# Performance work log

Measured on AMD Instinct MI355X. Metric: run time of the kernel, lower is better.

The kernel has to match this reference:

```python
import jax, jax.numpy as jnp
import numpy as np

B, D, C, H = 32768, 128, 128, 512
INTERVAL = 1.0
N_STEPS = 4
ENERGY_REG = 0.01
JACNORM_REG = 0.01


def setup_inputs() -> dict:
    key = jax.random.key(0)
    ks = jax.random.split(key, 8)
    return {
        "x": jax.random.normal(ks[0], (B, D), jnp.float32),
        "logpx": jnp.zeros((B,), jnp.float32),
        "cond": jax.random.normal(ks[1], (B, C), jnp.float32),
        "e": jax.random.normal(ks[2], (B, D), jnp.float32),  # Hutchinson noise
        "W1": jax.random.normal(ks[3], (D, H), jnp.float32) / np.sqrt(D),
        "Wc": jax.random.normal(ks[4], (C, H), jnp.float32) / np.sqrt(C),
        "bt": jax.random.normal(ks[5], (H,), jnp.float32) * 0.1,
        "b1": jnp.zeros((H,), jnp.float32),
        "W2": jax.random.normal(ks[6], (H, D), jnp.float32) / np.sqrt(H),
        "b2": jnp.zeros((D,), jnp.float32),
    }


def reference(x, logpx, cond, e, W1, Wc, bt, b1, W2, b2):
    def drift(t, xx):
        # func(t, x, cond): simple conditioned MLP drift
        h = jnp.tanh(xx @ W1 + cond @ Wc + t * bt + b1)
        return h @ W2 + b2

    def dynamics(t, xx):
        # Hutchinson divergence estimator: div = e^T (dF/dx) e via one VJP
        dx, vjp_fn = jax.vjp(lambda z: drift(t, z), xx)
        u = vjp_fn(e)[0]                      # [B, D] = e^T J
        div = jnp.sum(u * e, axis=1)          # [B]
        d_energy = jnp.sum(dx * dx) / xx.shape[0]
        d_jacnorm = jnp.sum(u * u) / xx.shape[0]
        return dx, -div, d_energy, d_jacnorm

    dt = INTERVAL / N_STEPS

    def rk4_step(carry, t0):
        xx, lp, en, jn = carry
        k1 = dynamics(t0, xx)
        k2 = dynamics(t0 + 0.5 * dt, xx + 0.5 * dt * k1[0])
        k3 = dynamics(t0 + 0.5 * dt, xx + 0.5 * dt * k2[0])
        k4 = dynamics(t0 + dt, xx + dt * k3[0])
        comb = lambda i: (k1[i] + 2.0 * k2[i] + 2.0 * k3[i] + k4[i]) / 6.0
        return (xx + dt * comb(0), lp + dt * comb(1), en + dt * comb(2), jn + dt * comb(3)), None

    ts = jnp.arange(N_STEPS, dtype=x.dtype) * dt
    init = (x, logpx, jnp.zeros((), x.dtype), jnp.zeros((), x.dtype))
    (y, logpy, energy, jacnorm), _ = jax.lax.scan(rk4_step, init, ts)

    # regularization: zero value, nonzero gradient (matches x - x.detach())
    reg = ENERGY_REG * (energy - jax.lax.stop_gradient(energy)) \
        + JACNORM_REG * (jacnorm - jax.lax.stop_gradient(jacnorm))
    return y, logpy + reg
```

## Files before the change

### kernel.cpp

```cpp
#include <hip/hip_runtime.h>

typedef unsigned short u16;
typedef unsigned int   u32;
typedef unsigned long long u64;
typedef __attribute__((ext_vector_type(8))) short bf16x8;
typedef __attribute__((ext_vector_type(4))) float f32x4;

#define MFMA16(A,B,C) __builtin_amdgcn_mfma_f32_16x16x32_bf16(A,B,C,0,0,0)
#define MFMAF8(A,B,C) __builtin_amdgcn_mfma_f32_16x16x32_fp8_fp8(A,B,C,0,0,0)

__device__ __forceinline__ u16 f2bf(float f){
    u32 u = __float_as_uint(f);
    u += 0x7fffu + ((u >> 16) & 1u);
    return (u16)(u >> 16);
}
__device__ __forceinline__ u32 pk2(float lo, float hi){
    return (u32)f2bf(lo) | ((u32)f2bf(hi) << 16);
}
__device__ __forceinline__ float upk(u32 u, int hi){
    return __uint_as_float(hi ? (u & 0xffff0000u) : (u << 16));
}
__device__ __forceinline__ float bf2f(u16 v){
    return __uint_as_float(((u32)v) << 16);
}
__device__ __forceinline__ float fast_tanh(float p){
    float e2 = __expf(2.f * p);
    return 1.f - __fdividef(2.f, e2 + 1.f);
}
__device__ __forceinline__ void gload16(const u16* g, u16* l){
    __builtin_amdgcn_global_load_lds((const __attribute__((address_space(1))) void*)g,
                                     (__attribute__((address_space(3))) void*)l, 16, 0, 0);
}

__global__ __launch_bounds__(256) void pack_weights_kernel(
    const float* __restrict__ W1, const float* __restrict__ W2,
    const float* __restrict__ Wc, u16* __restrict__ wp)
{
    int p = blockIdx.x * 256 + threadIdx.x;
    int which = p >> 16;
    int q = p & 65535;
    if (which == 1) return;
    if (which == 2){
        int j = q & 7, lane = (q >> 3) & 63;
        int nt = (q >> 9) & 7, lc = (q >> 12) & 15;
        int k = lc * 32 + (lane >> 4) * 8 + j;
        int n = nt * 16 + (lane & 15);
        float v = W2[k * 128 + n];
        u32 b = (u32)__builtin_amdgcn_cvt_pk_fp8_f32(v, 0.f, 0, 0) & 0xffu;
        ((unsigned char*)(wp + 131072))[q] = (unsigned char)b;
        return;
    }
    int j = q & 7, l = (q >> 3) & 63, t = (q >> 9) & 1;
    int ks = (q >> 10) & 3, c = (q >> 12) & 15;
    int l15v = l & 15, l4v = l >> 4;
    int k = 32 * ks + l4v * 8 + j;
    int n = 32 * c + 16 * t + l15v;
    float v = (which == 0) ? W1[k * 512 + n] : (which == 3) ? W2[n * 128 + k] : Wc[k * 512 + n];
    wp[p] = f2bf(v);
}

__global__ __launch_bounds__(512, 4) void cnf_mfma11_kernel(
    const float* __restrict__ x, const float* __restrict__ logpx,
    const float* __restrict__ cond, const float* __restrict__ e,
    const float* __restrict__ b1, const u16* __restrict__ wp,
    const float* __restrict__ bt, const float* __restrict__ b2,
    float* __restrict__ y_out, float* __restrict__ lp_out)
{
    __shared__ __align__(16) u16 s_w1[3][4096];
    __shared__ __align__(16) unsigned char s_w2s[4][4096];
    __shared__ __align__(16) u16 s_xx[4][16 * 136];
    __shared__ __align__(16) unsigned char s_hh8[4][2][16 * 40];
    __shared__ u16 s_bt[512];
    __shared__ float s_b2[128];
    __shared__ float s_red[4][2][16];

    const int tid = threadIdx.x, wave = tid >> 6, lane = tid & 63;
    const int l15 = lane & 15, l4 = lane >> 4;
    const int pair = wave >> 1, half = wave & 1;
    const int rbase = blockIdx.x * 64 + pair * 16;
    const int wlt4 = __builtin_amdgcn_readfirstlane((wave < 4) ? 1 : 0);

    const u16* W1p  = wp;
    const u16* W2Tp = wp + 196608;
    const u16* Wcp  = wp + 262144;
    const unsigned char* W2f8p = (const unsigned char*)(wp + 131072);

    auto stage_chunk = [&](int slot, int slot4, int cidx){
        gload16(W1p + cidx * 4096 + wave * 512 + lane * 8, &s_w1[slot][wave * 512 + lane * 8]);
        if (wave < 4)
            gload16((const u16*)(W2f8p + cidx * 4096 + wave * 1024 + lane * 16),
                    (u16*)&s_w2s[slot4][wave * 1024 + lane * 16]);
    };

    s_bt[tid] = f2bf(bt[tid]);
    if (tid < 128) s_b2[tid] = b2[tid];

    u32 base_pk[16][2], q_pk[16][2];

    {
        #pragma unroll
        for (int i = 0; i < 8; ++i){
            const int row = half * 8 + i;
            s_xx[pair][row * 136 + lane]      = f2bf(cond[(size_t)(rbase + row) * 128 + lane]);
            s_xx[pair][row * 136 + 64 + lane] = f2bf(cond[(size_t)(rbase + row) * 128 + 64 + lane]);
        }
        __syncthreads();
        bf16x8 cA[4];
        #pragma unroll
        for (int ks = 0; ks < 4; ++ks)
            cA[ks] = *(const bf16x8*)&s_xx[pair][l15 * 136 + ks * 32 + l4 * 8];
        __syncthreads();

        #pragma unroll 1
        for (int nc = 0; nc < 16; ++nc){
            gload16(Wcp + nc * 4096 + wave * 512 + lane * 8, &s_w1[0][wave * 512 + lane * 8]);
            __syncthreads();
            f32x4 ab = {0.f, 0.f, 0.f, 0.f};
            #pragma unroll
            for (int ks = 0; ks < 4; ++ks)
                ab = MFMA16(cA[ks], *(const bf16x8*)&s_w1[0][(ks * 2 + half) * 512 + lane * 8], ab);
            const float b1v = b1[nc * 32 + half * 16 + l15];
            base_pk[nc][0] = pk2(ab[0] + b1v, ab[1] + b1v);
            base_pk[nc][1] = pk2(ab[2] + b1v, ab[3] + b1v);
            __syncthreads();
        }
    }

    {
        #pragma unroll
        for (int i = 0; i < 8; ++i){
            const int row = half * 8 + i;
            s_xx[pair][row * 136 + lane]      = f2bf(e[(size_t)(rbase + row) * 128 + lane]);
            s_xx[pair][row * 136 + 64 + lane] = f2bf(e[(size_t)(rbase + row) * 128 + 64 + lane]);
        }
        __syncthreads();
        bf16x8 eA[4];
        #pragma unroll
        for (int ks = 0; ks < 4; ++ks)
            eA[ks] = *(const bf16x8*)&s_xx[pair][l15 * 136 + ks * 32 + l4 * 8];
        __syncthreads();

        #pragma unroll 1
        for (int nc = 0; nc < 16; ++nc){
            gload16(W1p  + nc * 4096 + wave * 512 + lane * 8, &s_w1[0][wave * 512 + lane * 8]);
            gload16(W2Tp + nc * 4096 + wave * 512 + lane * 8, &s_w1[1][wave * 512 + lane * 8]);
            __syncthreads();
            f32x4 ew = {0.f,0.f,0.f,0.f}, e2 = {0.f,0.f,0.f,0.f};
            #pragma unroll
            for (int ks = 0; ks < 4; ++ks){
                ew = MFMA16(eA[ks], *(const bf16x8*)&s_w1[0][(ks * 2 + half) * 512 + lane * 8], ew);
                e2 = MFMA16(eA[ks], *(const bf16x8*)&s_w1[1][(ks * 2 + half) * 512 + lane * 8], e2);
            }
            q_pk[nc][0] = pk2(ew[0] * e2[0], ew[1] * e2[1]);
            q_pk[nc][1] = pk2(ew[2] * e2[2], ew[3] * e2[3]);
            __syncthreads();
        }
    }

    u32 xs_pk[4][2];
    #pragma unroll
    for (int ntl = 0; ntl < 4; ++ntl)
        #pragma unroll
        for (int rr = 0; rr < 2; ++rr){
            const int row0 = rbase + l4 * 4 + 2 * rr;
            const int col = half * 64 + ntl * 16 + l15;
            const float a0 = x[(size_t)row0 * 128 + col];
            const float a1 = x[(size_t)(row0 + 1) * 128 + col];
            xs_pk[ntl][rr] = pk2(a0, a1);
            s_xx[pair][(l4 * 4 + 2 * rr) * 136 + col]     = (u16)(xs_pk[ntl][rr] & 0xffffu);
            s_xx[pair][(l4 * 4 + 2 * rr + 1) * 136 + col] = (u16)(xs_pk[ntl][rr] >> 16);
        }

    #pragma unroll
    for (int c = 0; c < 3; ++c) stage_chunk(c, c, c);
    if (wlt4) { asm volatile("s_waitcnt vmcnt(4) lgkmcnt(0)" ::: "memory"); }
    else      { asm volatile("s_waitcnt vmcnt(2) lgkmcnt(0)" ::: "memory"); }
    __builtin_amdgcn_sched_barrier(0);
    __builtin_amdgcn_s_barrier();
    asm volatile("" ::: "memory");

    f32x4 acc[4];
    u32 dxc_pk[4][2];
    float divacc[4] = {0.f, 0.f, 0.f, 0.f};
    #pragma unroll
    for (int ntl = 0; ntl < 4; ++ntl){
        acc[ntl] = {0.f, 0.f, 0.f, 0.f};
        dxc_pk[ntl][0] = 0u; dxc_pk[ntl][1] = 0u;
    }

    #pragma unroll 1
    for (int st = 0; st < 16; ++st){
        const int stg = st & 3;
        const float tcur = 0.25f * (float)(st >> 2) + ((stg == 0) ? 0.f : (stg == 3) ? 0.25f : 0.125f);
        const float wcur = (stg == 1 || stg == 2) ? 2.f : 1.f;

        #pragma unroll 1
        for (int lc = 0; lc < 16; ++lc){
            const int c = st * 16 + lc;
            const int slot = c % 3;

            {
                const float btv = bf2f(s_bt[lc * 32 + half * 16 + l15]);
                f32x4 pa, pb = {0.f, 0.f, 0.f, 0.f};
                pa[0] = upk(base_pk[lc][0], 0) + tcur * btv;
                pa[1] = upk(base_pk[lc][0], 1) + tcur * btv;
                pa[2] = upk(base_pk[lc][1], 0) + tcur * btv;
                pa[3] = upk(base_pk[lc][1], 1) + tcur * btv;
                bf16x8 xxA0 = *(const bf16x8*)&s_xx[pair][l15 * 136 +  0 + l4 * 8];
                bf16x8 xxA1 = *(const bf16x8*)&s_xx[pair][l15 * 136 + 32 + l4 * 8];
                bf16x8 xxA2 = *(const bf16x8*)&s_xx[pair][l15 * 136 + 64 + l4 * 8];
                bf16x8 xxA3 = *(const bf16x8*)&s_xx[pair][l15 * 136 + 96 + l4 * 8];
                pa = MFMA16(xxA0, *(const bf16x8*)&s_w1[slot][(0 * 2 + half) * 512 + lane * 8], pa);
                pb = MFMA16(xxA1, *(const bf16x8*)&s_w1[slot][(1 * 2 + half) * 512 + lane * 8], pb);
                pa = MFMA16(xxA2, *(const bf16x8*)&s_w1[slot][(2 * 2 + half) * 512 + lane * 8], pa);
                pb = MFMA16(xxA3, *(const bf16x8*)&s_w1[slot][(3 * 2 + half) * 512 + lane * 8], pb);
                #pragma unroll
                for (int r = 0; r < 4; ++r){
                    const float h = fast_tanh(pa[r] + pb[r]);
                    divacc[r] += wcur * (1.f - h * h) * upk(q_pk[lc][r >> 1], r & 1);
                    const u32 hb = (u32)__builtin_amdgcn_cvt_pk_fp8_f32(h, h, 0, 0) & 0xffu;
                    s_hh8[pair][c & 1][(l4 * 4 + r) * 40 + half * 16 + l15] = (unsigned char)hb;
                }
            }

            if (wlt4) { asm volatile("s_waitcnt vmcnt(2) lgkmcnt(0)" ::: "memory"); }
            else      { asm volatile("s_waitcnt vmcnt(1) lgkmcnt(0)" ::: "memory"); }
            __builtin_amdgcn_sched_barrier(0);
            __builtin_amdgcn_s_barrier();
            asm volatile("" ::: "memory");

            stage_chunk((c + 3) % 3, (c + 3) & 3, (c + 3) & 15);

            {
                const u64 hf8 = *(const u64*)&s_hh8[pair][c & 1][l15 * 40 + l4 * 8];
                #pragma unroll
                for (int ntl = 0; ntl < 4; ++ntl){
                    const u64 wf8 = *(const u64*)&s_w2s[c & 3][(half * 4 + ntl) * 512 + lane * 8];
                    acc[ntl] = MFMAF8((long)hf8, (long)wf8, acc[ntl]);
                }
            }
        }

        const float adt = (stg == 2) ? 0.25f : 0.125f;
        #pragma unroll
        for (int ntl = 0; ntl < 4; ++ntl){
            const float b2v = s_b2[half * 64 + ntl * 16 + l15];
            #pragma unroll
            for (int rr = 0; rr < 2; ++rr){
                const float d0 = acc[ntl][2 * rr] + b2v;
                const float d1 = acc[ntl][2 * rr + 1] + b2v;
                const float c0 = upk(dxc_pk[ntl][rr], 0) + wcur * d0;
                const float c1 = upk(dxc_pk[ntl][rr], 1) + wcur * d1;
                const float x00 = upk(xs_pk[ntl][rr], 0);
                const float x01 = upk(xs_pk[ntl][rr], 1);
                float xn0, xn1;
                if (stg < 3){
                    dxc_pk[ntl][rr] = pk2(c0, c1);
                    xn0 = x00 + adt * d0;
                    xn1 = x01 + adt * d1;
                } else {
                    dxc_pk[ntl][rr] = 0u;
                    xn0 = x00 + (0.25f / 6.f) * c0;
                    xn1 = x01 + (0.25f / 6.f) * c1;
                    xs_pk[ntl][rr] = pk2(xn0, xn1);
                }
                const int col = half * 64 + ntl * 16 + l15;
                s_xx[pair][(l4 * 4 + 2 * rr) * 136 + col]     = f2bf(xn0);
                s_xx[pair][(l4 * 4 + 2 * rr + 1) * 136 + col] = f2bf(xn1);
                if (st == 15){
                    y_out[(size_t)(rbase + l4 * 4 + 2 * rr) * 128 + col]     = xn0;
                    y_out[(size_t)(rbase + l4 * 4 + 2 * rr + 1) * 128 + col] = xn1;
                }
                acc[ntl][2 * rr] = 0.f; acc[ntl][2 * rr + 1] = 0.f;
            }
        }

        asm volatile("s_waitcnt lgkmcnt(0)" ::: "memory");
        __builtin_amdgcn_sched_barrier(0);
        __builtin_amdgcn_s_barrier();
        asm volatile("" ::: "memory");
    }

    #pragma unroll
    for (int r = 0; r < 4; ++r){
        float d = divacc[r];
        d += __shfl_xor(d, 1);
        d += __shfl_xor(d, 2);
        d += __shfl_xor(d, 4);
        d += __shfl_xor(d, 8);
        if (l15 == 0) s_red[pair][half][l4 * 4 + r] = d;
    }
    __syncthreads();
    if (half == 0 && l15 == 0){
        #pragma unroll
        for (int r = 0; r < 4; ++r){
            const int row16 = l4 * 4 + r;
            const int row = rbase + row16;
            lp_out[row] = logpx[row] - (0.25f / 6.f) * (s_red[pair][0][row16] + s_red[pair][1][row16]);
        }
    }
}

extern "C" void kernel_launch(void* const* d_in, const int* in_sizes, int n_in,
                              void* d_out, int out_size, void* d_ws, size_t ws_size,
                              hipStream_t stream) {
    const float* x     = (const float*)d_in[0];
    const float* logpx = (const float*)d_in[1];
    const float* cond  = (const float*)d_in[2];
    const float* e     = (const float*)d_in[3];
    const float* W1    = (const float*)d_in[4];
    const float* Wc    = (const float*)d_in[5];
    const float* bt    = (const float*)d_in[6];
    const float* b1    = (const float*)d_in[7];
    const float* W2    = (const float*)d_in[8];
    const float* b2    = (const float*)d_in[9];

    u16* wp = (u16*)d_ws;
    float* y_out  = (float*)d_out;
    float* lp_out = y_out + (size_t)32768 * 128;

    hipLaunchKernelGGL(pack_weights_kernel, dim3(1280), dim3(256), 0, stream, W1, W2, Wc, wp);
    hipLaunchKernelGGL(cnf_mfma11_kernel, dim3(512), dim3(512), 0, stream,
                       x, logpx, cond, e, b1, wp, bt, b2, y_out, lp_out);
}
```

Measured before the change: 383.8 us.

## Regroup waves into 4-wave row groups with 64-wide hidden chunks and double buffering

```diff
diff --git a/kernel.cpp b/kernel.cpp
--- a/kernel.cpp
+++ b/kernel.cpp
@@ -3,6 +3,7 @@
 typedef unsigned short u16;
 typedef unsigned int   u32;
 typedef unsigned long long u64;
+typedef unsigned char  u8;
 typedef __attribute__((ext_vector_type(8))) short bf16x8;
 typedef __attribute__((ext_vector_type(4))) float f32x4;
 
@@ -37,89 +38,93 @@
     const float* __restrict__ Wc, u16* __restrict__ wp)
 {
     int p = blockIdx.x * 256 + threadIdx.x;
-    int which = p >> 16;
-    int q = p & 65535;
-    if (which == 1) return;
-    if (which == 2){
-        int j = q & 7, lane = (q >> 3) & 63;
-        int nt = (q >> 9) & 7, lc = (q >> 12) & 15;
-        int k = lc * 32 + (lane >> 4) * 8 + j;
-        int n = nt * 16 + (lane & 15);
-        float v = W2[k * 128 + n];
+    if (p < 196608){
+        int which = p >> 16;
+        int q = p & 65535;
+        int c = q >> 13, w = q & 8191;
+        int j = w & 7, l = (w >> 3) & 63, t = (w >> 9) & 3, ks = (w >> 11) & 3;
+        int k = 32 * ks + (l >> 4) * 8 + j;
+        int n = 64 * c + 16 * t + (l & 15);
+        float v = (which == 0) ? W1[k * 512 + n]
+                : (which == 1) ? W2[n * 128 + k]
+                :                Wc[k * 512 + n];
+        wp[p] = f2bf(v);
+    } else {
+        int q = p - 196608;
+        int c = q >> 13, w = q & 8191;
+        int j = w & 7, lane = (w >> 3) & 63, nt = (w >> 9) & 7, ksl = (w >> 12) & 1;
+        int kh = 64 * c + 32 * ksl + (lane >> 4) * 8 + j;
+        int nd = 16 * nt + (lane & 15);
+        float v = W2[kh * 128 + nd];
         u32 b = (u32)__builtin_amdgcn_cvt_pk_fp8_f32(v, 0.f, 0, 0) & 0xffu;
-        ((unsigned char*)(wp + 131072))[q] = (unsigned char)b;
-        return;
-    }
-    int j = q & 7, l = (q >> 3) & 63, t = (q >> 9) & 1;
-    int ks = (q >> 10) & 3, c = (q >> 12) & 15;
-    int l15v = l & 15, l4v = l >> 4;
-    int k = 32 * ks + l4v * 8 + j;
-    int n = 32 * c + 16 * t + l15v;
-    float v = (which == 0) ? W1[k * 512 + n] : (which == 3) ? W2[n * 128 + k] : Wc[k * 512 + n];
-    wp[p] = f2bf(v);
-}
-
-__global__ __launch_bounds__(512, 4) void cnf_mfma11_kernel(
+        ((u8*)(wp + 196608))[q] = (u8)b;
+    }
+}
+
+__global__ __launch_bounds__(512, 4) void cnf_mfma12_kernel(
     const float* __restrict__ x, const float* __restrict__ logpx,
     const float* __restrict__ cond, const float* __restrict__ e,
     const float* __restrict__ b1, const u16* __restrict__ wp,
     const float* __restrict__ bt, const float* __restrict__ b2,
     float* __restrict__ y_out, float* __restrict__ lp_out)
 {
-    __shared__ __align__(16) u16 s_w1[3][4096];
-    __shared__ __align__(16) unsigned char s_w2s[4][4096];
-    __shared__ __align__(16) u16 s_xx[4][16 * 136];
-    __shared__ __align__(16) unsigned char s_hh8[4][2][16 * 40];
+    __shared__ __align__(16) u16 s_w1[2][8192];
+    __shared__ __align__(16) u8  s_w2[2][8192];
+    __shared__ __align__(16) u16 s_xx[2][16 * 132];
+    __shared__ __align__(16) u8  s_hh8[2][2][16 * 72];
     __shared__ u16 s_bt[512];
     __shared__ float s_b2[128];
-    __shared__ float s_red[4][2][16];
+    __shared__ float s_red[2][4][16];
 
     const int tid = threadIdx.x, wave = tid >> 6, lane = tid & 63;
     const int l15 = lane & 15, l4 = lane >> 4;
-    const int pair = wave >> 1, half = wave & 1;
-    const int rbase = blockIdx.x * 64 + pair * 16;
-    const int wlt4 = __builtin_amdgcn_readfirstlane((wave < 4) ? 1 : 0);
+    const int g = wave >> 2, wq = wave & 3;
+    const int gtid = tid & 255;
+    const int rbase = blockIdx.x * 32 + g * 16;
 
     const u16* W1p  = wp;
-    const u16* W2Tp = wp + 196608;
-    const u16* Wcp  = wp + 262144;
-    const unsigned char* W2f8p = (const unsigned char*)(wp + 131072);
-
-    auto stage_chunk = [&](int slot, int slot4, int cidx){
-        gload16(W1p + cidx * 4096 + wave * 512 + lane * 8, &s_w1[slot][wave * 512 + lane * 8]);
-        if (wave < 4)
-            gload16((const u16*)(W2f8p + cidx * 4096 + wave * 1024 + lane * 16),
-                    (u16*)&s_w2s[slot4][wave * 1024 + lane * 16]);
+    const u16* W2Tp = wp + 65536;
+    const u16* Wcp  = wp + 131072;
+    const u8*  W2f8p = (const u8*)(wp + 196608);
+
+    auto stage_chunk = [&](int cidx){
+        const int slot = cidx & 1;
+        const u16* src = W1p + cidx * 8192 + tid * 8;
+        gload16(src,        &s_w1[slot][tid * 8]);
+        gload16(src + 4096, &s_w1[slot][4096 + tid * 8]);
+        gload16((const u16*)(W2f8p + cidx * 8192 + tid * 16), (u16*)&s_w2[slot][tid * 16]);
     };
 
     s_bt[tid] = f2bf(bt[tid]);
     if (tid < 128) s_b2[tid] = b2[tid];
 
-    u32 base_pk[16][2], q_pk[16][2];
+    u32 base_pk[8][2], q_pk[8][2];
 
     {
         #pragma unroll
         for (int i = 0; i < 8; ++i){
-            const int row = half * 8 + i;
-            s_xx[pair][row * 136 + lane]      = f2bf(cond[(size_t)(rbase + row) * 128 + lane]);
-            s_xx[pair][row * 136 + 64 + lane] = f2bf(cond[(size_t)(rbase + row) * 128 + 64 + lane]);
+            const int elem = i * 256 + gtid;
+            const int row = elem >> 7, col = elem & 127;
+            s_xx[g][row * 132 + col] = f2bf(cond[(size_t)(rbase + row) * 128 + col]);
         }
         __syncthreads();
         bf16x8 cA[4];
         #pragma unroll
         for (int ks = 0; ks < 4; ++ks)
-            cA[ks] = *(const bf16x8*)&s_xx[pair][l15 * 136 + ks * 32 + l4 * 8];
+            cA[ks] = *(const bf16x8*)&s_xx[g][l15 * 132 + ks * 32 + l4 * 8];
         __syncthreads();
 
         #pragma unroll 1
-        for (int nc = 0; nc < 16; ++nc){
-            gload16(Wcp + nc * 4096 + wave * 512 + lane * 8, &s_w1[0][wave * 512 + lane * 8]);
+        for (int nc = 0; nc < 8; ++nc){
+            const u16* src = Wcp + nc * 8192 + tid * 8;
+            gload16(src,        &s_w1[0][tid * 8]);
+            gload16(src + 4096, &s_w1[0][4096 + tid * 8]);
             __syncthreads();
             f32x4 ab = {0.f, 0.f, 0.f, 0.f};
             #pragma unroll
             for (int ks = 0; ks < 4; ++ks)
-                ab = MFMA16(cA[ks], *(const bf16x8*)&s_w1[0][(ks * 2 + half) * 512 + lane * 8], ab);
-            const float b1v = b1[nc * 32 + half * 16 + l15];
+                ab = MFMA16(cA[ks], *(const bf16x8*)&s_w1[0][(ks * 4 + wq) * 512 + lane * 8], ab);
+            const float b1v = b1[nc * 64 + wq * 16 + l15];
             base_pk[nc][0] = pk2(ab[0] + b1v, ab[1] + b1v);
             base_pk[nc][1] = pk2(ab[2] + b1v, ab[3] + b1v);
             __syncthreads();
@@ -129,27 +134,31 @@
     {
         #pragma unroll
         for (int i = 0; i < 8; ++i){
-            const int row = half * 8 + i;
-            s_xx[pair][row * 136 + lane]      = f2bf(e[(size_t)(rbase + row) * 128 + lane]);
-            s_xx[pair][row * 136 + 64 + lane] = f2bf(e[(size_t)(rbase + row) * 128 + 64 + lane]);
+            const int elem = i * 256 + gtid;
+            const int row = elem >> 7, col = elem & 127;
+            s_xx[g][row * 132 + col] = f2bf(e[(size_t)(rbase + row) * 128 + col]);
         }
         __syncthreads();
         bf16x8 eA[4];
         #pragma unroll
         for (int ks = 0; ks < 4; ++ks)
-            eA[ks] = *(const bf16x8*)&s_xx[pair][l15 * 136 + ks * 32 + l4 * 8];
+            eA[ks] = *(const bf16x8*)&s_xx[g][l15 * 132 + ks * 32 + l4 * 8];
         __syncthreads();
 
         #pragma unroll 1
-        for (int nc = 0; nc < 16; ++nc){
-            gload16(W1p  + nc * 4096 + wave * 512 + lane * 8, &s_w1[0][wave * 512 + lane * 8]);
-            gload16(W2Tp + nc * 4096 + wave * 512 + lane * 8, &s_w1[1][wave * 512 + lane * 8]);
+        for (int nc = 0; nc < 8; ++nc){
+            const u16* s1 = W1p  + nc * 8192 + tid * 8;
+            const u16* s2 = W2Tp + nc * 8192 + tid * 8;
+            gload16(s1,        &s_w1[0][tid * 8]);
+            gload16(s1 + 4096, &s_w1[0][4096 + tid * 8]);
+            gload16(s2,        &s_w1[1][tid * 8]);
+            gload16(s2 + 4096, &s_w1[1][4096 + tid * 8]);
             __syncthreads();
             f32x4 ew = {0.f,0.f,0.f,0.f}, e2 = {0.f,0.f,0.f,0.f};
             #pragma unroll
             for (int ks = 0; ks < 4; ++ks){
-                ew = MFMA16(eA[ks], *(const bf16x8*)&s_w1[0][(ks * 2 + half) * 512 + lane * 8], ew);
-                e2 = MFMA16(eA[ks], *(const bf16x8*)&s_w1[1][(ks * 2 + half) * 512 + lane * 8], e2);
+                ew = MFMA16(eA[ks], *(const bf16x8*)&s_w1[0][(ks * 4 + wq) * 512 + lane * 8], ew);
+                e2 = MFMA16(eA[ks], *(const bf16x8*)&s_w1[1][(ks * 4 + wq) * 512 + lane * 8], e2);
             }
             q_pk[nc][0] = pk2(ew[0] * e2[0], ew[1] * e2[1]);
             q_pk[nc][1] = pk2(ew[2] * e2[2], ew[3] * e2[3]);
@@ -157,33 +166,32 @@
         }
     }
 
-    u32 xs_pk[4][2];
+    u32 xs_pk[2][2];
     #pragma unroll
-    for (int ntl = 0; ntl < 4; ++ntl)
+    for (int ntl = 0; ntl < 2; ++ntl)
         #pragma unroll
         for (int rr = 0; rr < 2; ++rr){
             const int row0 = rbase + l4 * 4 + 2 * rr;
-            const int col = half * 64 + ntl * 16 + l15;
+            const int col = wq * 32 + ntl * 16 + l15;
             const float a0 = x[(size_t)row0 * 128 + col];
             const float a1 = x[(size_t)(row0 + 1) * 128 + col];
             xs_pk[ntl][rr] = pk2(a0, a1);
-            s_xx[pair][(l4 * 4 + 2 * rr) * 136 + col]     = (u16)(xs_pk[ntl][rr] & 0xffffu);
-            s_xx[pair][(l4 * 4 + 2 * rr + 1) * 136 + col] = (u16)(xs_pk[ntl][rr] >> 16);
-        }
-
-    #pragma unroll
-    for (int c = 0; c < 3; ++c) stage_chunk(c, c, c);
-    if (wlt4) { asm volatile("s_waitcnt vmcnt(4) lgkmcnt(0)" ::: "memory"); }
-    else      { asm volatile("s_waitcnt vmcnt(2) lgkmcnt(0)" ::: "memory"); }
+            s_xx[g][(l4 * 4 + 2 * rr) * 132 + col]     = (u16)(xs_pk[ntl][rr] & 0xffffu);
+            s_xx[g][(l4 * 4 + 2 * rr + 1) * 132 + col] = (u16)(xs_pk[ntl][rr] >> 16);
+        }
+
+    stage_chunk(0);
+    stage_chunk(1);
+    asm volatile("s_waitcnt vmcnt(3) lgkmcnt(0)" ::: "memory");
     __builtin_amdgcn_sched_barrier(0);
     __builtin_amdgcn_s_barrier();
     asm volatile("" ::: "memory");
 
-    f32x4 acc[4];
-    u32 dxc_pk[4][2];
+    f32x4 acc[2];
+    u32 dxc_pk[2][2];
     float divacc[4] = {0.f, 0.f, 0.f, 0.f};
     #pragma unroll
-    for (int ntl = 0; ntl < 4; ++ntl){
+    for (int ntl = 0; ntl < 2; ++ntl){
         acc[ntl] = {0.f, 0.f, 0.f, 0.f};
         dxc_pk[ntl][0] = 0u; dxc_pk[ntl][1] = 0u;
     }
@@ -195,56 +203,62 @@
         const float wcur = (stg == 1 || stg == 2) ? 2.f : 1.f;
 
         #pragma unroll 1
-        for (int lc = 0; lc < 16; ++lc){
-            const int c = st * 16 + lc;
-            const int slot = c % 3;
+        for (int lc = 0; lc < 8; ++lc){
+            const int c = st * 8 + lc;
+            const int slot = c & 1;
+            u64 wf8[2][2];
 
             {
-                const float btv = bf2f(s_bt[lc * 32 + half * 16 + l15]);
+                const float btv = bf2f(s_bt[lc * 64 + wq * 16 + l15]);
                 f32x4 pa, pb = {0.f, 0.f, 0.f, 0.f};
                 pa[0] = upk(base_pk[lc][0], 0) + tcur * btv;
                 pa[1] = upk(base_pk[lc][0], 1) + tcur * btv;
                 pa[2] = upk(base_pk[lc][1], 0) + tcur * btv;
                 pa[3] = upk(base_pk[lc][1], 1) + tcur * btv;
-                bf16x8 xxA0 = *(const bf16x8*)&s_xx[pair][l15 * 136 +  0 + l4 * 8];
-                bf16x8 xxA1 = *(const bf16x8*)&s_xx[pair][l15 * 136 + 32 + l4 * 8];
-                bf16x8 xxA2 = *(const bf16x8*)&s_xx[pair][l15 * 136 + 64 + l4 * 8];
-                bf16x8 xxA3 = *(const bf16x8*)&s_xx[pair][l15 * 136 + 96 + l4 * 8];
-                pa = MFMA16(xxA0, *(const bf16x8*)&s_w1[slot][(0 * 2 + half) * 512 + lane * 8], pa);
-                pb = MFMA16(xxA1, *(const bf16x8*)&s_w1[slot][(1 * 2 + half) * 512 + lane * 8], pb);
-                pa = MFMA16(xxA2, *(const bf16x8*)&s_w1[slot][(2 * 2 + half) * 512 + lane * 8], pa);
-                pb = MFMA16(xxA3, *(const bf16x8*)&s_w1[slot][(3 * 2 + half) * 512 + lane * 8], pb);
+                bf16x8 xxA0 = *(const bf16x8*)&s_xx[g][l15 * 132 +  0 + l4 * 8];
+                bf16x8 xxA1 = *(const bf16x8*)&s_xx[g][l15 * 132 + 32 + l4 * 8];
+                bf16x8 xxA2 = *(const bf16x8*)&s_xx[g][l15 * 132 + 64 + l4 * 8];
+                bf16x8 xxA3 = *(const bf16x8*)&s_xx[g][l15 * 132 + 96 + l4 * 8];
+                pa = MFMA16(xxA0, *(const bf16x8*)&s_w1[slot][(0 * 4 + wq) * 512 + lane * 8], pa);
+                pb = MFMA16(xxA1, *(const bf16x8*)&s_w1[slot][(1 * 4 + wq) * 512 + lane * 8], pb);
+                pa = MFMA16(xxA2, *(const bf16x8*)&s_w1[slot][(2 * 4 + wq) * 512 + lane * 8], pa);
+                pb = MFMA16(xxA3, *(const bf16x8*)&s_w1[slot][(3 * 4 + wq) * 512 + lane * 8], pb);
+
+                #pragma unroll
+                for (int ksl = 0; ksl < 2; ++ksl)
+                    #pragma unroll
+                    for (int ntl = 0; ntl < 2; ++ntl)
+                        wf8[ksl][ntl] = *(const u64*)&s_w2[slot][(ksl * 8 + wq * 2 + ntl) * 512 + lane * 8];
+
                 #pragma unroll
                 for (int r = 0; r < 4; ++r){
                     const float h = fast_tanh(pa[r] + pb[r]);
                     divacc[r] += wcur * (1.f - h * h) * upk(q_pk[lc][r >> 1], r & 1);
                     const u32 hb = (u32)__builtin_amdgcn_cvt_pk_fp8_f32(h, h, 0, 0) & 0xffu;
-                    s_hh8[pair][c & 1][(l4 * 4 + r) * 40 + half * 16 + l15] = (unsigned char)hb;
+                    s_hh8[g][c & 1][(l4 * 4 + r) * 72 + wq * 16 + l15] = (u8)hb;
                 }
             }
 
-            if (wlt4) { asm volatile("s_waitcnt vmcnt(2) lgkmcnt(0)" ::: "memory"); }
-            else      { asm volatile("s_waitcnt vmcnt(1) lgkmcnt(0)" ::: "memory"); }
+            asm volatile("s_waitcnt vmcnt(0) lgkmcnt(0)" ::: "memory");
             __builtin_amdgcn_sched_barrier(0);
             __builtin_amdgcn_s_barrier();
             asm volatile("" ::: "memory");
 
-            stage_chunk((c + 3) % 3, (c + 3) & 3, (c + 3) & 15);
-
-            {
-                const u64 hf8 = *(const u64*)&s_hh8[pair][c & 1][l15 * 40 + l4 * 8];
+            stage_chunk((c + 2) & 7);
+
+            #pragma unroll
+            for (int ksl = 0; ksl < 2; ++ksl){
+                const u64 hf8 = *(const u64*)&s_hh8[g][c & 1][l15 * 72 + ksl * 32 + l4 * 8];
                 #pragma unroll
-                for (int ntl = 0; ntl < 4; ++ntl){
-                    const u64 wf8 = *(const u64*)&s_w2s[c & 3][(half * 4 + ntl) * 512 + lane * 8];
-                    acc[ntl] = MFMAF8((long)hf8, (long)wf8, acc[ntl]);
-                }
+                for (int ntl = 0; ntl < 2; ++ntl)
+                    acc[ntl] = MFMAF8((long)hf8, (long)wf8[ksl][ntl], acc[ntl]);
             }
         }
 
         const float adt = (stg == 2) ? 0.25f : 0.125f;
         #pragma unroll
-        for (int ntl = 0; ntl < 4; ++ntl){
-            const float b2v = s_b2[half * 64 + ntl * 16 + l15];
+        for (int ntl = 0; ntl < 2; ++ntl){
+            const float b2v = s_b2[wq * 32 + ntl * 16 + l15];
             #pragma unroll
             for (int rr = 0; rr < 2; ++rr){
                 const float d0 = acc[ntl][2 * rr] + b2v;
@@ -264,9 +278,9 @@
                     xn1 = x01 + (0.25f / 6.f) * c1;
                     xs_pk[ntl][rr] = pk2(xn0, xn1);
                 }
-                const int col = half * 64 + ntl * 16 + l15;
-                s_xx[pair][(l4 * 4 + 2 * rr) * 136 + col]     = f2bf(xn0);
-                s_xx[pair][(l4 * 4 + 2 * rr + 1) * 136 + col] = f2bf(xn1);
+                const int col = wq * 32 + ntl * 16 + l15;
+                s_xx[g][(l4 * 4 + 2 * rr) * 132 + col]     = f2bf(xn0);
+                s_xx[g][(l4 * 4 + 2 * rr + 1) * 132 + col] = f2bf(xn1);
                 if (st == 15){
                     y_out[(size_t)(rbase + l4 * 4 + 2 * rr) * 128 + col]     = xn0;
                     y_out[(size_t)(rbase + l4 * 4 + 2 * rr + 1) * 128 + col] = xn1;
@@ -288,15 +302,17 @@
         d += __shfl_xor(d, 2);
         d += __shfl_xor(d, 4);
         d += __shfl_xor(d, 8);
-        if (l15 == 0) s_red[pair][half][l4 * 4 + r] = d;
+        if (l15 == 0) s_red[g][wq][l4 * 4 + r] = d;
     }
     __syncthreads();
-    if (half == 0 && l15 == 0){
+    if (wq == 0 && l15 == 0){
         #pragma unroll
         for (int r = 0; r < 4; ++r){
             const int row16 = l4 * 4 + r;
             const int row = rbase + row16;
-            lp_out[row] = logpx[row] - (0.25f / 6.f) * (s_red[pair][0][row16] + s_red[pair][1][row16]);
+            const float s = s_red[g][0][row16] + s_red[g][1][row16]
+                          + s_red[g][2][row16] + s_red[g][3][row16];
+            lp_out[row] = logpx[row] - (0.25f / 6.f) * s;
         }
     }
 }
@@ -319,7 +335,7 @@
     float* y_out  = (float*)d_out;
     float* lp_out = y_out + (size_t)32768 * 128;
 
-    hipLaunchKernelGGL(pack_weights_kernel, dim3(1280), dim3(256), 0, stream, W1, W2, Wc, wp);
-    hipLaunchKernelGGL(cnf_mfma11_kernel, dim3(512), dim3(512), 0, stream,
+    hipLaunchKernelGGL(pack_weights_kernel, dim3(1024), dim3(256), 0, stream, W1, W2, Wc, wp);
+    hipLaunchKernelGGL(cnf_mfma12_kernel, dim3(1024), dim3(512), 0, stream,
                        x, logpx, cond, e, b1, wp, bt, b2, y_out, lp_out);
 }
```

After: 380.7 us. About the same (-0.8%).
